# Kernel tuning notes

Measured on AMD Instinct MI355X. Metric: run time of the kernel, lower is better.

## Reference

```python
import jax, jax.numpy as jnp
import numpy as np

N, E, G = 100000, 400000, 2000
F_IN, HID, H = 74, 64, 4
HID4 = HID * H           # 256, per-node feature after flatten(1)
POOL = 3 * HID4          # 768, concat(mean, max, sum)
OUT = 128
NEG_SLOPE = 0.2          # DGL GATConv default LeakyReLU slope


def setup_inputs() -> dict:
    key = jax.random.key(0)
    ks = jax.random.split(key, 20)
    p = lambda k, shape: (jax.random.normal(k, shape, jnp.float32) * 0.05)
    inp = {
        "node_feat": jax.random.normal(ks[0], (N, F_IN), jnp.float32),
        "src": jax.random.randint(ks[1], (E,), 0, N, jnp.int32),
        "dst": jax.random.randint(ks[2], (E,), 0, N, jnp.int32),
        # every graph gets exactly N//G nodes (sorted, non-empty segments)
        "graph_ids": jnp.arange(N, dtype=jnp.int32) // (N // G),
        "enc_W": p(ks[3], (F_IN, HID)), "enc_b": jnp.zeros((HID,), jnp.float32),
    }
    in_dims = [HID, HID4, HID4]
    for l in range(3):
        inp[f"W{l}"] = p(ks[4 + 4 * l], (in_dims[l], H * HID))
        inp[f"al{l}"] = p(ks[5 + 4 * l], (H, HID))
        inp[f"ar{l}"] = p(ks[6 + 4 * l], (H, HID))
        inp[f"b{l}"] = jnp.zeros((H * HID,), jnp.float32)
    inp["r1_W"] = p(ks[16], (POOL, HID)); inp["r1_b"] = jnp.zeros((HID,), jnp.float32)
    inp["r2_W"] = p(ks[17], (HID, OUT)); inp["r2_b"] = jnp.zeros((OUT,), jnp.float32)
    return inp


def _gat_layer(h, src, dst, W, al, ar, b):
    # DGL GATConv (eval mode: dropouts are identity), activation=ReLU
    z = (h @ W).reshape(N, H, HID)                       # [N,H,O]
    el = jnp.einsum("nho,ho->nh", z, al)                 # [N,H]
    er = jnp.einsum("nho,ho->nh", z, ar)
    e = jax.nn.leaky_relu(el[src] + er[dst], NEG_SLOPE)  # [E,H]
    # segment softmax over incoming edges of each dst node, per head
    m = jax.ops.segment_max(e, dst, num_segments=N)      # [N,H]
    ex = jnp.exp(e - m[dst])
    s = jax.ops.segment_sum(ex, dst, num_segments=N)     # [N,H]
    a = ex / s[dst]                                      # [E,H]
    out = jax.ops.segment_sum(z[src] * a[:, :, None], dst, num_segments=N)
    out = out + b.reshape(1, H, HID)                     # GATConv bias
    return jax.nn.relu(out).reshape(N, HID4)             # flatten(1)


def reference(node_feat, src, dst, graph_ids, enc_W, enc_b,
              W0, al0, ar0, b0, W1, al1, ar1, b1, W2, al2, ar2, b2,
              r1_W, r1_b, r2_W, r2_b):
    h = node_feat @ enc_W + enc_b                        # node encoder
    h = _gat_layer(h, src, dst, W0, al0, ar0, b0)
    h = _gat_layer(h, src, dst, W1, al1, ar1, b1)
    h = _gat_layer(h, src, dst, W2, al2, ar2, b2)
    # multi-pool readout: mean / max / sum over nodes of each graph
    h_sum = jax.ops.segment_sum(h, graph_ids, num_segments=G)
    cnt = jax.ops.segment_sum(jnp.ones((N, 1), h.dtype), graph_ids, num_segments=G)
    h_mean = h_sum / cnt
    h_max = jax.ops.segment_max(h, graph_ids, num_segments=G)
    hg = jnp.concatenate([h_mean, h_max, h_sum], axis=1)  # [G, 3*HID4]
    hg = jax.nn.relu(hg @ r1_W + r1_b)
    return hg @ r2_W + r2_b                              # [G, OUT]
```

## Files before the change

kernel.cpp:

```cpp
#include <hip/hip_runtime.h>

#define N_NODES 100000
#define N_EDGES 400000
#define N_GRAPHS 2000
#define F_IN 74
#define ENC_KP 96
#define HID 64
#define NHEAD 4
#define HID4 256
#define OUT_DIM 128
#define NODES_PER_G 50

typedef __attribute__((ext_vector_type(8))) short short8;
typedef __attribute__((ext_vector_type(4))) float f32x4;

__device__ inline ushort f2bf(float f) {
  union { float f; unsigned u; } v; v.f = f;
  unsigned u = v.u;
  return (ushort)((u + 0x7FFFu + ((u >> 16) & 1u)) >> 16);
}
__device__ inline float bf2f(ushort b) {
  union { unsigned u; float f; } v; v.u = ((unsigned)b) << 16;
  return v.f;
}
__device__ inline float leaky(float x) { return x >= 0.f ? x : 0.2f * x; }

__device__ inline void glds16(const ushort* g, ushort* l) {
  __builtin_amdgcn_global_load_lds(
      (const __attribute__((address_space(1))) void*)g,
      (__attribute__((address_space(3))) void*)l, 16, 0, 0);
}

__global__ __launch_bounds__(256) void k_count(const int* __restrict__ dst,
                                               int* __restrict__ off) {
  int e = blockIdx.x * 256 + threadIdx.x;
  if (e < N_EDGES) atomicAdd(&off[dst[e] + 1], 1);
}

__global__ __launch_bounds__(256) void k_scan1(int* __restrict__ data, int n,
                                               int* __restrict__ blksum) {
  __shared__ int sh[256];
  int t = threadIdx.x;
  int base = blockIdx.x * 1024 + t * 4;
  int v0 = (base + 0 < n) ? data[base + 0] : 0;
  int v1 = (base + 1 < n) ? data[base + 1] : 0;
  int v2 = (base + 2 < n) ? data[base + 2] : 0;
  int v3 = (base + 3 < n) ? data[base + 3] : 0;
  v1 += v0; v2 += v1; v3 += v2;
  int tot = v3;
  sh[t] = tot;
  __syncthreads();
  for (int o = 1; o < 256; o <<= 1) {
    int x = (t >= o) ? sh[t - o] : 0;
    __syncthreads();
    sh[t] += x;
    __syncthreads();
  }
  int excl = sh[t] - tot;
  if (base + 0 < n) data[base + 0] = v0 + excl;
  if (base + 1 < n) data[base + 1] = v1 + excl;
  if (base + 2 < n) data[base + 2] = v2 + excl;
  if (base + 3 < n) data[base + 3] = v3 + excl;
  if (t == 255) blksum[blockIdx.x] = sh[255];
}

__global__ __launch_bounds__(256) void k_scan2(int* __restrict__ blksum, int nb) {
  __shared__ int sh[256];
  int t = threadIdx.x;
  sh[t] = (t < nb) ? blksum[t] : 0;
  __syncthreads();
  for (int o = 1; o < 256; o <<= 1) {
    int x = (t >= o) ? sh[t - o] : 0;
    __syncthreads();
    sh[t] += x;
    __syncthreads();
  }
  if (t < nb) blksum[t] = sh[t];
}

__global__ __launch_bounds__(256) void k_scan3(int* __restrict__ data, int n,
                                               const int* __restrict__ blksum) {
  int b = blockIdx.x;
  if (b == 0) return;
  int add = blksum[b - 1];
  int base = b * 1024 + threadIdx.x * 4;
  for (int j = 0; j < 4; ++j)
    if (base + j < n) data[base + j] += add;
}

__global__ __launch_bounds__(256) void k_scatter(const int* __restrict__ dst,
                                                 const int* __restrict__ src,
                                                 const int* __restrict__ off,
                                                 int* __restrict__ cursor,
                                                 int* __restrict__ srcs) {
  int e = blockIdx.x * 256 + threadIdx.x;
  if (e >= N_EDGES) return;
  int d = dst[e];
  int pos = off[d] + atomicAdd(&cursor[d], 1);
  srcs[pos] = src[e];
}

__global__ __launch_bounds__(256) void k_sortseg(const int* __restrict__ off,
                                                 int* __restrict__ srcs) {
  int n = blockIdx.x * 256 + threadIdx.x;
  if (n >= N_NODES) return;
  int beg = off[n], end = off[n + 1];
  for (int i = beg + 1; i < end; ++i) {
    int key = srcs[i];
    int j = i - 1;
    while (j >= beg && srcs[j] > key) { srcs[j + 1] = srcs[j]; --j; }
    srcs[j + 1] = key;
  }
}

__global__ __launch_bounds__(256) void k_wt_enc(const float* __restrict__ W,
                                                ushort* __restrict__ Wte) {
  int idx = blockIdx.x * 256 + threadIdx.x;
  if (idx >= HID * ENC_KP) return;
  int col = idx / ENC_KP;
  int k = idx - col * ENC_KP;
  ushort v = 0;
  if (k < F_IN) v = f2bf(W[(size_t)k * HID + col]);
  Wte[idx] = v;
}

__global__ __launch_bounds__(256) void k_enc_mfma(const float* __restrict__ nf,
                                                  const ushort* __restrict__ Bt,
                                                  const float* __restrict__ bias,
                                                  ushort* __restrict__ Cb) {
  __shared__ ushort As[128][104];
  __shared__ ushort Bs[64][104];
  int t = threadIdx.x;
  int lane = t & 63;
  int wid = t >> 6;
  int brow = blockIdx.x * 128;

  for (int i = t; i < 128 * ENC_KP; i += 256) {
    int r = i / ENC_KP;
    int c = i - r * ENC_KP;
    int gr = brow + r;
    float v = 0.f;
    if (gr < N_NODES && c < F_IN) v = nf[(size_t)gr * F_IN + c];
    As[r][c] = f2bf(v);
  }
  if (t < 128) {
    int r = t >> 1;
    int o = (t & 1) * 48;
#pragma unroll
    for (int i = 0; i < 6; ++i)
      *(int4*)&Bs[r][o + i * 8] = *(const int4*)(Bt + (size_t)r * ENC_KP + o + i * 8);
  }
  __syncthreads();

  int fr = lane & 15;
  int ko = (lane >> 4) * 8;
  f32x4 acc[2][4];
#pragma unroll
  for (int m = 0; m < 2; ++m)
#pragma unroll
    for (int n = 0; n < 4; ++n) acc[m][n] = (f32x4)(0.f);

#pragma unroll
  for (int ks = 0; ks < 3; ++ks) {
    short8 a[2], b[4];
#pragma unroll
    for (int m = 0; m < 2; ++m) a[m] = *(const short8*)&As[wid * 32 + m * 16 + fr][ks * 32 + ko];
#pragma unroll
    for (int n = 0; n < 4; ++n) b[n] = *(const short8*)&Bs[n * 16 + fr][ks * 32 + ko];
#pragma unroll
    for (int m = 0; m < 2; ++m)
#pragma unroll
      for (int n = 0; n < 4; ++n)
        acc[m][n] = __builtin_amdgcn_mfma_f32_16x16x32_bf16(a[m], b[n], acc[m][n], 0, 0, 0);
  }

  int r0 = (lane >> 4) * 4;
  int cc = lane & 15;
#pragma unroll
  for (int m = 0; m < 2; ++m) {
#pragma unroll
    for (int j = 0; j < 4; ++j) {
      int row = brow + wid * 32 + m * 16 + r0 + j;
      if (row >= N_NODES) continue;
#pragma unroll
      for (int n = 0; n < 4; ++n) {
        int col = n * 16 + cc;
        Cb[(size_t)row * HID + col] = f2bf(acc[m][n][j] + bias[col]);
      }
    }
  }
}

template <int K>
__global__ __launch_bounds__(256) void k_wt(const float* __restrict__ W,
                                            ushort* __restrict__ Wt) {
  int idx = blockIdx.x * 256 + threadIdx.x;
  if (idx >= K * HID4) return;
  int k = idx >> 8;
  int n = idx & 255;
  Wt[(size_t)n * K + k] = f2bf(W[idx]);
}

template <int K>
__global__ __launch_bounds__(256) void k_gemm_mfma(const ushort* __restrict__ A,
                                                   const ushort* __restrict__ Bt,
                                                   ushort* __restrict__ Cb,
                                                   const float* __restrict__ al,
                                                   const float* __restrict__ ar,
                                                   float* __restrict__ el,
                                                   float* __restrict__ er,
                                                   int n_rows) {
  __shared__ __align__(16) ushort As[2][128 * 32];
  __shared__ __align__(16) ushort Bs[2][128 * 32];
  int t = threadIdx.x;
  int lane = t & 63;
  int wid = t >> 6;
  int wr = wid >> 1, wc = wid & 1;
  int brow = blockIdx.x * 128;
  int bcol = blockIdx.y * 128;

  f32x4 acc[4][4];
#pragma unroll
  for (int m = 0; m < 4; ++m)
#pragma unroll
    for (int n = 0; n < 4; ++n) acc[m][n] = (f32x4)(0.f);

  int srow0 = (wid * 2 + 0) * 16 + (lane >> 2);
  int srow1 = (wid * 2 + 1) * 16 + (lane >> 2);
  int skc = (lane & 3) * 8;
  int ga0 = brow + srow0; if (ga0 > n_rows - 1) ga0 = n_rows - 1;
  int ga1 = brow + srow1; if (ga1 > n_rows - 1) ga1 = n_rows - 1;
  const ushort* pa0 = A + (size_t)ga0 * K + skc;
  const ushort* pa1 = A + (size_t)ga1 * K + skc;
  const ushort* pb0 = Bt + (size_t)(bcol + srow0) * K + skc;
  const ushort* pb1 = Bt + (size_t)(bcol + srow1) * K + skc;
  int lo0 = (wid * 2 + 0) * 512;
  int lo1 = (wid * 2 + 1) * 512;

  int fr = lane & 15;
  int ko = (lane >> 4) * 8;

  glds16(pa0, &As[0][lo0]);
  glds16(pa1, &As[0][lo1]);
  glds16(pb0, &Bs[0][lo0]);
  glds16(pb1, &Bs[0][lo1]);
  __syncthreads();
  int cur = 0;

  for (int k0 = 0; k0 < K; k0 += 32) {
    if (k0 + 32 < K) {
      glds16(pa0 + k0 + 32, &As[cur ^ 1][lo0]);
      glds16(pa1 + k0 + 32, &As[cur ^ 1][lo1]);
      glds16(pb0 + k0 + 32, &Bs[cur ^ 1][lo0]);
      glds16(pb1 + k0 + 32, &Bs[cur ^ 1][lo1]);
    }
    short8 a[4], b[4];
#pragma unroll
    for (int m = 0; m < 4; ++m)
      a[m] = *(const short8*)(&As[cur][0] + (wr * 64 + m * 16 + fr) * 32 + ko);
#pragma unroll
    for (int n = 0; n < 4; ++n)
      b[n] = *(const short8*)(&Bs[cur][0] + (wc * 64 + n * 16 + fr) * 32 + ko);
#pragma unroll
    for (int m = 0; m < 4; ++m)
#pragma unroll
      for (int n = 0; n < 4; ++n)
        acc[m][n] = __builtin_amdgcn_mfma_f32_16x16x32_bf16(a[m], b[n], acc[m][n], 0, 0, 0);
    __syncthreads();
    cur ^= 1;
  }

  int r0 = (lane >> 4) * 4;
  int cc = lane & 15;
  int q = blockIdx.y * 2 + wc;
  float alr[4], arr[4];
#pragma unroll
  for (int n = 0; n < 4; ++n) {
    int col = bcol + wc * 64 + n * 16 + cc;
    alr[n] = al[col];
    arr[n] = ar[col];
  }
#pragma unroll
  for (int m = 0; m < 4; ++m) {
#pragma unroll
    for (int j = 0; j < 4; ++j) {
      float pl = 0.f, pr = 0.f;
#pragma unroll
      for (int n = 0; n < 4; ++n) {
        pl = fmaf(acc[m][n][j], alr[n], pl);
        pr = fmaf(acc[m][n][j], arr[n], pr);
      }
#pragma unroll
      for (int o = 1; o < 16; o <<= 1) {
        pl += __shfl_xor(pl, o, 64);
        pr += __shfl_xor(pr, o, 64);
      }
      int row = brow + wr * 64 + m * 16 + r0 + j;
      if (row >= n_rows) continue;
      if (cc == 0) {
        el[(size_t)row * NHEAD + q] = pl;
        er[(size_t)row * NHEAD + q] = pr;
      }
#pragma unroll
      for (int n = 0; n < 4; ++n)
        Cb[(size_t)row * HID4 + bcol + wc * 64 + n * 16 + cc] = f2bf(acc[m][n][j]);
    }
  }
}

__global__ __launch_bounds__(256) void k_agg(const ushort* __restrict__ zb,
                                             const float* __restrict__ el,
                                             const float* __restrict__ er,
                                             const int* __restrict__ off,
                                             const int* __restrict__ srcs,
                                             const float* __restrict__ bias,
                                             ushort* __restrict__ outb) {
  int w = (blockIdx.x * 256 + threadIdx.x) >> 6;
  int lane = threadIdx.x & 63;
  int half = lane >> 5;
  int li = lane & 31;
  int n = w * 2 + half;
  if (n >= N_NODES) return;
  int h = li >> 3;
  int c = li * 8;
  int beg = off[n], end = off[n + 1];
  float erh = er[(size_t)n * NHEAD + h];

  float s = 0.f;
  float acc[8] = {0.f, 0.f, 0.f, 0.f, 0.f, 0.f, 0.f, 0.f};

  float e0 = 0.f, e1 = 0.f, e2 = 0.f;
  int4 z0 = make_int4(0, 0, 0, 0), z1 = z0, z2 = z0;
  if (beg < end) {
    int sn = srcs[beg];
    e0 = el[(size_t)sn * NHEAD + h];
    z0 = *(const int4*)(zb + (size_t)sn * HID4 + c);
  }
  if (beg + 1 < end) {
    int sn = srcs[beg + 1];
    e1 = el[(size_t)sn * NHEAD + h];
    z1 = *(const int4*)(zb + (size_t)sn * HID4 + c);
  }
  if (beg + 2 < end) {
    int sn = srcs[beg + 2];
    e2 = el[(size_t)sn * NHEAD + h];
    z2 = *(const int4*)(zb + (size_t)sn * HID4 + c);
  }
  int sn3 = (beg + 3 < end) ? srcs[beg + 3] : 0;

  for (int p = beg; p < end; ++p) {
    float ev = e0;
    int4 zv = z0;
    e0 = e1; z0 = z1;
    e1 = e2; z1 = z2;
    int sn4 = (p + 4 < end) ? srcs[p + 4] : 0;
    if (p + 3 < end) {
      e2 = el[(size_t)sn3 * NHEAD + h];
      z2 = *(const int4*)(zb + (size_t)sn3 * HID4 + c);
    } else {
      e2 = 0.f;
    }
    sn3 = sn4;
    float pv = __expf(leaky(ev + erh));
    s += pv;
    const ushort* us = (const ushort*)&zv;
#pragma unroll
    for (int j = 0; j < 8; ++j) acc[j] = fmaf(pv, bf2f(us[j]), acc[j]);
  }
  float inv = (s > 0.f) ? 1.f / s : 0.f;
  float4 b40 = *(const float4*)(bias + c);
  float4 b41 = *(const float4*)(bias + c + 4);
  float bb[8] = {b40.x, b40.y, b40.z, b40.w, b41.x, b41.y, b41.z, b41.w};
  int4 ov;
  ushort* os = (ushort*)&ov;
#pragma unroll
  for (int j = 0; j < 8; ++j) os[j] = f2bf(fmaxf(acc[j] * inv + bb[j], 0.f));
  *(int4*)(outb + (size_t)n * HID4 + c) = ov;
}

__global__ __launch_bounds__(256) void k_pool_mlp(const ushort* __restrict__ h,
                                                  const float* __restrict__ r1W,
                                                  const float* __restrict__ r1b,
                                                  const float* __restrict__ r2W,
                                                  const float* __restrict__ r2b,
                                                  float* __restrict__ out) {
  __shared__ float pooled[3 * HID4];
  __shared__ float part[4][HID];
  __shared__ float mid[HID];
  int g = blockIdx.x;
  int t = threadIdx.x;
  const ushort* base = h + (size_t)g * NODES_PER_G * HID4;
  float sum = 0.f, mx = -1e30f;
  for (int i = 0; i < NODES_PER_G; ++i) {
    float v = bf2f(base[(size_t)i * HID4 + t]);
    sum += v;
    mx = fmaxf(mx, v);
  }
  pooled[t] = sum / (float)NODES_PER_G;
  pooled[HID4 + t] = mx;
  pooled[2 * HID4 + t] = sum;
  __syncthreads();
  {
    int o = t & 63, chunk = t >> 6;
    float acc = 0.f;
    int k0 = chunk * 192;
    for (int k = k0; k < k0 + 192; ++k) acc = fmaf(pooled[k], r1W[k * HID + o], acc);
    part[chunk][o] = acc;
  }
  __syncthreads();
  if (t < HID) {
    float acc = r1b[t] + part[0][t] + part[1][t] + part[2][t] + part[3][t];
    mid[t] = fmaxf(acc, 0.f);
  }
  __syncthreads();
  if (t < OUT_DIM) {
    float acc = r2b[t];
    for (int k = 0; k < HID; ++k) acc = fmaf(mid[k], r2W[k * OUT_DIM + t], acc);
    out[(size_t)g * OUT_DIM + t] = acc;
  }
}

extern "C" void kernel_launch(void* const* d_in, const int* in_sizes, int n_in,
                              void* d_out, int out_size, void* d_ws, size_t ws_size,
                              hipStream_t stream) {
  const float* node_feat = (const float*)d_in[0];
  const int* src = (const int*)d_in[1];
  const int* dst = (const int*)d_in[2];
  const float* enc_W = (const float*)d_in[4];
  const float* enc_b = (const float*)d_in[5];
  const float* Wl[3] = {(const float*)d_in[6], (const float*)d_in[10], (const float*)d_in[14]};
  const float* all[3] = {(const float*)d_in[7], (const float*)d_in[11], (const float*)d_in[15]};
  const float* arl[3] = {(const float*)d_in[8], (const float*)d_in[12], (const float*)d_in[16]};
  const float* bl[3] = {(const float*)d_in[9], (const float*)d_in[13], (const float*)d_in[17]};
  const float* r1W = (const float*)d_in[18];
  const float* r1b = (const float*)d_in[19];
  const float* r2W = (const float*)d_in[20];
  const float* r2b = (const float*)d_in[21];
  float* out = (float*)d_out;

  char* p = (char*)d_ws;
  auto alloc = [&](size_t bytes) {
    void* r = (void*)p;
    p += (bytes + 255) & ~(size_t)255;
    return r;
  };
  int* off = (int*)alloc((N_NODES + 1) * sizeof(int));
  int* cursor = (int*)alloc(N_NODES * sizeof(int));
  int* srcs = (int*)alloc(N_EDGES * sizeof(int));
  int* blksum = (int*)alloc(256 * sizeof(int));
  float* el = (float*)alloc((size_t)N_NODES * NHEAD * sizeof(float));
  float* er = (float*)alloc((size_t)N_NODES * NHEAD * sizeof(float));
  ushort* Qb = (ushort*)alloc((size_t)N_NODES * HID4 * sizeof(ushort));
  ushort* Pb = (ushort*)alloc((size_t)N_NODES * HID4 * sizeof(ushort));
  ushort* Wt = (ushort*)alloc((size_t)HID4 * HID4 * sizeof(ushort));
  ushort* Wte = (ushort*)alloc((size_t)HID * ENC_KP * sizeof(ushort));

  hipMemsetAsync(off, 0, (N_NODES + 1) * sizeof(int), stream);
  hipMemsetAsync(cursor, 0, N_NODES * sizeof(int), stream);
  k_count<<<(N_EDGES + 255) / 256, 256, 0, stream>>>(dst, off);
  const int SCAN_N = N_NODES + 1;
  const int NB = (SCAN_N + 1023) / 1024;
  k_scan1<<<NB, 256, 0, stream>>>(off, SCAN_N, blksum);
  k_scan2<<<1, 256, 0, stream>>>(blksum, NB);
  k_scan3<<<NB, 256, 0, stream>>>(off, SCAN_N, blksum);
  k_scatter<<<(N_EDGES + 255) / 256, 256, 0, stream>>>(dst, src, off, cursor, srcs);
  k_sortseg<<<(N_NODES + 255) / 256, 256, 0, stream>>>(off, srcs);

  k_wt_enc<<<(HID * ENC_KP + 255) / 256, 256, 0, stream>>>(enc_W, Wte);
  k_enc_mfma<<<(N_NODES + 127) / 128, 256, 0, stream>>>(node_feat, Wte, enc_b, Pb);

  dim3 ggrid((N_NODES + 127) / 128, HID4 / 128);
  const int AGG_WAVES = (N_NODES + 1) / 2;
  const int AGG_BLOCKS = (AGG_WAVES + 3) / 4;
  for (int l = 0; l < 3; ++l) {
    if (l == 0) {
      k_wt<HID><<<(HID * HID4 + 255) / 256, 256, 0, stream>>>(Wl[0], Wt);
      k_gemm_mfma<HID><<<ggrid, 256, 0, stream>>>(Pb, Wt, Qb, all[0], arl[0], el, er, N_NODES);
    } else {
      k_wt<HID4><<<(HID4 * HID4 + 255) / 256, 256, 0, stream>>>(Wl[l], Wt);
      k_gemm_mfma<HID4><<<ggrid, 256, 0, stream>>>(Pb, Wt, Qb, all[l], arl[l], el, er, N_NODES);
    }
    k_agg<<<AGG_BLOCKS, 256, 0, stream>>>(Qb, el, er, off, srcs, bl[l], Pb);
  }

  k_pool_mlp<<<N_GRAPHS, 256, 0, stream>>>(Pb, r1W, r1b, r2W, r2b, out);
}
```

Measured before the change: 378.9 us.

## Widen GEMM tile to full 256 columns and give aggregation 16 lanes per node

The projection GEMM now uses 512-thread blocks that cover all 256 output columns per 128-row tile. This removes the second grid column, so each A tile is loaded once instead of twice. The aggregation kernel now assigns 16 lanes per node instead of 32, with each lane handling 16 features through two 16-byte gathers, giving 4 nodes per wave. The trade-offs are more LDS and registers per block, which may lower occupancy, and fewer threads per node in the gather-heavy aggregation loop.

```diff
diff --git a/kernel.cpp b/kernel.cpp
--- a/kernel.cpp
+++ b/kernel.cpp
@@ -202,7 +202,7 @@
 }
 
 template <int K>
-__global__ __launch_bounds__(256) void k_gemm_mfma(const ushort* __restrict__ A,
+__global__ __launch_bounds__(512) void k_gemm_mfma(const ushort* __restrict__ A,
                                                    const ushort* __restrict__ Bt,
                                                    ushort* __restrict__ Cb,
                                                    const float* __restrict__ al,
@@ -211,13 +211,13 @@
                                                    float* __restrict__ er,
                                                    int n_rows) {
   __shared__ __align__(16) ushort As[2][128 * 32];
-  __shared__ __align__(16) ushort Bs[2][128 * 32];
+  __shared__ __align__(16) ushort Bs[2][256 * 32];
   int t = threadIdx.x;
   int lane = t & 63;
   int wid = t >> 6;
-  int wr = wid >> 1, wc = wid & 1;
+  int wr = wid >> 2;
+  int wc = wid & 3;
   int brow = blockIdx.x * 128;
-  int bcol = blockIdx.y * 128;
 
   f32x4 acc[4][4];
 #pragma unroll
@@ -225,34 +225,30 @@
 #pragma unroll
     for (int n = 0; n < 4; ++n) acc[m][n] = (f32x4)(0.f);
 
-  int srow0 = (wid * 2 + 0) * 16 + (lane >> 2);
-  int srow1 = (wid * 2 + 1) * 16 + (lane >> 2);
+  int lr = lane >> 2;
   int skc = (lane & 3) * 8;
-  int ga0 = brow + srow0; if (ga0 > n_rows - 1) ga0 = n_rows - 1;
-  int ga1 = brow + srow1; if (ga1 > n_rows - 1) ga1 = n_rows - 1;
-  const ushort* pa0 = A + (size_t)ga0 * K + skc;
-  const ushort* pa1 = A + (size_t)ga1 * K + skc;
-  const ushort* pb0 = Bt + (size_t)(bcol + srow0) * K + skc;
-  const ushort* pb1 = Bt + (size_t)(bcol + srow1) * K + skc;
-  int lo0 = (wid * 2 + 0) * 512;
-  int lo1 = (wid * 2 + 1) * 512;
+  int gaA = brow + wid * 16 + lr; if (gaA > n_rows - 1) gaA = n_rows - 1;
+  const ushort* paA = A + (size_t)gaA * K + skc;
+  const ushort* pbB0 = Bt + (size_t)(wid * 32 + lr) * K + skc;
+  const ushort* pbB1 = Bt + (size_t)(wid * 32 + 16 + lr) * K + skc;
+  int loA = wid * 512;
+  int loB0 = (wid * 2 + 0) * 512;
+  int loB1 = (wid * 2 + 1) * 512;
 
   int fr = lane & 15;
   int ko = (lane >> 4) * 8;
 
-  glds16(pa0, &As[0][lo0]);
-  glds16(pa1, &As[0][lo1]);
-  glds16(pb0, &Bs[0][lo0]);
-  glds16(pb1, &Bs[0][lo1]);
+  glds16(paA, &As[0][loA]);
+  glds16(pbB0, &Bs[0][loB0]);
+  glds16(pbB1, &Bs[0][loB1]);
   __syncthreads();
   int cur = 0;
 
   for (int k0 = 0; k0 < K; k0 += 32) {
     if (k0 + 32 < K) {
-      glds16(pa0 + k0 + 32, &As[cur ^ 1][lo0]);
-      glds16(pa1 + k0 + 32, &As[cur ^ 1][lo1]);
-      glds16(pb0 + k0 + 32, &Bs[cur ^ 1][lo0]);
-      glds16(pb1 + k0 + 32, &Bs[cur ^ 1][lo1]);
+      glds16(paA + k0 + 32, &As[cur ^ 1][loA]);
+      glds16(pbB0 + k0 + 32, &Bs[cur ^ 1][loB0]);
+      glds16(pbB1 + k0 + 32, &Bs[cur ^ 1][loB1]);
     }
     short8 a[4], b[4];
 #pragma unroll
@@ -272,11 +268,11 @@
 
   int r0 = (lane >> 4) * 4;
   int cc = lane & 15;
-  int q = blockIdx.y * 2 + wc;
+  int q = wc;
   float alr[4], arr[4];
 #pragma unroll
   for (int n = 0; n < 4; ++n) {
-    int col = bcol + wc * 64 + n * 16 + cc;
+    int col = wc * 64 + n * 16 + cc;
     alr[n] = al[col];
     arr[n] = ar[col];
   }
@@ -303,7 +299,7 @@
       }
 #pragma unroll
       for (int n = 0; n < 4; ++n)
-        Cb[(size_t)row * HID4 + bcol + wc * 64 + n * 16 + cc] = f2bf(acc[m][n][j]);
+        Cb[(size_t)row * HID4 + wc * 64 + n * 16 + cc] = f2bf(acc[m][n][j]);
     }
   }
 }
@@ -317,65 +313,78 @@
                                              ushort* __restrict__ outb) {
   int w = (blockIdx.x * 256 + threadIdx.x) >> 6;
   int lane = threadIdx.x & 63;
-  int half = lane >> 5;
-  int li = lane & 31;
-  int n = w * 2 + half;
+  int n = w * 4 + (lane >> 4);
+  int li = lane & 15;
   if (n >= N_NODES) return;
-  int h = li >> 3;
-  int c = li * 8;
+  int h = li >> 2;
+  int c = li * 16;
   int beg = off[n], end = off[n + 1];
   float erh = er[(size_t)n * NHEAD + h];
 
   float s = 0.f;
-  float acc[8] = {0.f, 0.f, 0.f, 0.f, 0.f, 0.f, 0.f, 0.f};
+  float acc[16];
+#pragma unroll
+  for (int j = 0; j < 16; ++j) acc[j] = 0.f;
 
   float e0 = 0.f, e1 = 0.f, e2 = 0.f;
-  int4 z0 = make_int4(0, 0, 0, 0), z1 = z0, z2 = z0;
+  int4 za0 = make_int4(0, 0, 0, 0), zb0 = za0;
+  int4 za1 = za0, zb1 = za0, za2 = za0, zb2 = za0;
   if (beg < end) {
     int sn = srcs[beg];
     e0 = el[(size_t)sn * NHEAD + h];
-    z0 = *(const int4*)(zb + (size_t)sn * HID4 + c);
+    const ushort* zp = zb + (size_t)sn * HID4 + c;
+    za0 = *(const int4*)zp; zb0 = *(const int4*)(zp + 8);
   }
   if (beg + 1 < end) {
     int sn = srcs[beg + 1];
     e1 = el[(size_t)sn * NHEAD + h];
-    z1 = *(const int4*)(zb + (size_t)sn * HID4 + c);
+    const ushort* zp = zb + (size_t)sn * HID4 + c;
+    za1 = *(const int4*)zp; zb1 = *(const int4*)(zp + 8);
   }
   if (beg + 2 < end) {
     int sn = srcs[beg + 2];
     e2 = el[(size_t)sn * NHEAD + h];
-    z2 = *(const int4*)(zb + (size_t)sn * HID4 + c);
-  }
-  int sn3 = (beg + 3 < end) ? srcs[beg + 3] : 0;
+    const ushort* zp = zb + (size_t)sn * HID4 + c;
+    za2 = *(const int4*)zp; zb2 = *(const int4*)(zp + 8);
+  }
 
   for (int p = beg; p < end; ++p) {
     float ev = e0;
-    int4 zv = z0;
-    e0 = e1; z0 = z1;
-    e1 = e2; z1 = z2;
-    int sn4 = (p + 4 < end) ? srcs[p + 4] : 0;
+    int4 va = za0, vb = zb0;
+    e0 = e1; za0 = za1; zb0 = zb1;
+    e1 = e2; za1 = za2; zb1 = zb2;
     if (p + 3 < end) {
-      e2 = el[(size_t)sn3 * NHEAD + h];
-      z2 = *(const int4*)(zb + (size_t)sn3 * HID4 + c);
-    } else {
-      e2 = 0.f;
+      int sn = srcs[p + 3];
+      e2 = el[(size_t)sn * NHEAD + h];
+      const ushort* zp = zb + (size_t)sn * HID4 + c;
+      za2 = *(const int4*)zp; zb2 = *(const int4*)(zp + 8);
     }
-    sn3 = sn4;
     float pv = __expf(leaky(ev + erh));
     s += pv;
-    const ushort* us = (const ushort*)&zv;
-#pragma unroll
-    for (int j = 0; j < 8; ++j) acc[j] = fmaf(pv, bf2f(us[j]), acc[j]);
+    const ushort* ua = (const ushort*)&va;
+    const ushort* ub = (const ushort*)&vb;
+#pragma unroll
+    for (int j = 0; j < 8; ++j) acc[j] = fmaf(pv, bf2f(ua[j]), acc[j]);
+#pragma unroll
+    for (int j = 0; j < 8; ++j) acc[8 + j] = fmaf(pv, bf2f(ub[j]), acc[8 + j]);
   }
   float inv = (s > 0.f) ? 1.f / s : 0.f;
-  float4 b40 = *(const float4*)(bias + c);
-  float4 b41 = *(const float4*)(bias + c + 4);
-  float bb[8] = {b40.x, b40.y, b40.z, b40.w, b41.x, b41.y, b41.z, b41.w};
-  int4 ov;
-  ushort* os = (ushort*)&ov;
-#pragma unroll
-  for (int j = 0; j < 8; ++j) os[j] = f2bf(fmaxf(acc[j] * inv + bb[j], 0.f));
-  *(int4*)(outb + (size_t)n * HID4 + c) = ov;
+  float bb[16];
+#pragma unroll
+  for (int j = 0; j < 16; j += 4) {
+    float4 b4 = *(const float4*)(bias + c + j);
+    bb[j] = b4.x; bb[j + 1] = b4.y; bb[j + 2] = b4.z; bb[j + 3] = b4.w;
+  }
+  int4 ov0, ov1;
+  ushort* os0 = (ushort*)&ov0;
+  ushort* os1 = (ushort*)&ov1;
+#pragma unroll
+  for (int j = 0; j < 8; ++j) os0[j] = f2bf(fmaxf(acc[j] * inv + bb[j], 0.f));
+#pragma unroll
+  for (int j = 0; j < 8; ++j) os1[j] = f2bf(fmaxf(acc[8 + j] * inv + bb[8 + j], 0.f));
+  ushort* op = outb + (size_t)n * HID4 + c;
+  *(int4*)op = ov0;
+  *(int4*)(op + 8) = ov1;
 }
 
 __global__ __launch_bounds__(256) void k_pool_mlp(const ushort* __restrict__ h,
@@ -469,16 +478,15 @@
   k_wt_enc<<<(HID * ENC_KP + 255) / 256, 256, 0, stream>>>(enc_W, Wte);
   k_enc_mfma<<<(N_NODES + 127) / 128, 256, 0, stream>>>(node_feat, Wte, enc_b, Pb);
 
-  dim3 ggrid((N_NODES + 127) / 128, HID4 / 128);
-  const int AGG_WAVES = (N_NODES + 1) / 2;
-  const int AGG_BLOCKS = (AGG_WAVES + 3) / 4;
+  const int GGRID = (N_NODES + 127) / 128;
+  const int AGG_BLOCKS = ((N_NODES + 3) / 4 + 3) / 4;
   for (int l = 0; l < 3; ++l) {
     if (l == 0) {
       k_wt<HID><<<(HID * HID4 + 255) / 256, 256, 0, stream>>>(Wl[0], Wt);
-      k_gemm_mfma<HID><<<ggrid, 256, 0, stream>>>(Pb, Wt, Qb, all[0], arl[0], el, er, N_NODES);
+      k_gemm_mfma<HID><<<GGRID, 512, 0, stream>>>(Pb, Wt, Qb, all[0], arl[0], el, er, N_NODES);
     } else {
       k_wt<HID4><<<(HID4 * HID4 + 255) / 256, 256, 0, stream>>>(Wl[l], Wt);
-      k_gemm_mfma<HID4><<<ggrid, 256, 0, stream>>>(Pb, Wt, Qb, all[l], arl[l], el, er, N_NODES);
+      k_gemm_mfma<HID4><<<GGRID, 512, 0, stream>>>(Pb, Wt, Qb, all[l], arl[l], el, er, N_NODES);
     }
     k_agg<<<AGG_BLOCKS, 256, 0, stream>>>(Qb, el, er, off, srcs, bl[l], Pb);
   }
```

After: 385.4 us. About the same (+1.7%).
